# Kernel optimization log

Measured on AMD Instinct MI355X. Metric: run time of the kernel, lower is better.

Reference implementation:

```python
import jax, jax.numpy as jnp
import numpy as np

B, S, D = 4, 2048, 768
H = 12
DH = D // H  # 64


def setup_inputs() -> dict:
    key = jax.random.key(0)
    ks = jax.random.split(key, 6)
    scale = 0.02
    return {
        "hidden_states": jax.random.normal(ks[0], (B, S, D), dtype=jnp.float32),
        "Wq": jax.random.normal(ks[1], (D, D), dtype=jnp.float32) * scale,
        "bq": jnp.zeros((D,), dtype=jnp.float32),
        "Wk": jax.random.normal(ks[2], (D, D), dtype=jnp.float32) * scale,
        "bk": jnp.zeros((D,), dtype=jnp.float32),
        "Wv": jax.random.normal(ks[3], (D, D), dtype=jnp.float32) * scale,
        "bv": jnp.zeros((D,), dtype=jnp.float32),
        "Wo": jax.random.normal(ks[4], (D, D), dtype=jnp.float32) * scale,
        "bo": jnp.zeros((D,), dtype=jnp.float32),
        "w_mix": jnp.ones((2,), dtype=jnp.float32),
    }


def reference(hidden_states, Wq, bq, Wk, bk, Wv, bv, Wo, bo, w_mix):
    # Q/K/V projections, then split heads: [B,S,D] -> [B,H,S,DH]
    def split_heads(x):
        return x.reshape(B, S, H, DH).transpose(0, 2, 1, 3)

    q = split_heads(hidden_states @ Wq.T + bq)
    k = split_heads(hidden_states @ Wk.T + bk)
    v = split_heads(hidden_states @ Wv.T + bv)

    # [B,H,S,S] attention scores
    scores = jnp.einsum("bhqd,bhkd->bhqk", q, k) / jnp.sqrt(jnp.float32(DH))

    attn_soft = jax.nn.softmax(scores, axis=-1)
    attn_relu2 = jnp.square(jax.nn.relu(scores))
    mix = jax.nn.softmax(w_mix)  # exp(w)/sum(exp(w))
    attn = attn_soft * mix[0] + attn_relu2 * mix[1]
    # dropout rate 0.0 (inference) -> identity

    ctx = jnp.einsum("bhqk,bhkd->bhqd", attn, v)
    ctx = ctx.transpose(0, 2, 1, 3).reshape(B, S, D)
    out = ctx @ Wo.T + bo
    return out
```

## Files before the change

kernel.cpp:

```cpp
#include <hip/hip_runtime.h>

#define DEV __device__ __forceinline__

typedef __attribute__((ext_vector_type(8))) short short8;
typedef __attribute__((ext_vector_type(4))) float f32x4;
typedef __attribute__((ext_vector_type(2))) unsigned int u32x2;
typedef __attribute__((ext_vector_type(4))) unsigned int u32x4;

constexpr int Dm = 768;
constexpr int Sn = 2048;
constexpr int Bn = 4;
constexpr int Hn = 12;
constexpr int Mn = Bn * Sn;

constexpr float kQScale = 0.18033688011112043f;
constexpr float kR2Fix  = 0.4804530139182014f;

DEV unsigned short f32_to_bf16(float f) {
  unsigned int u = __float_as_uint(f);
  u = (u + 0x7fffu + ((u >> 16) & 1u)) >> 16;
  return (unsigned short)u;
}

DEV unsigned cvt_pk_bf16(float lo, float hi) {
  unsigned d;
  asm("v_cvt_pk_bf16_f32 %0, %1, %2" : "=v"(d) : "v"(lo), "v"(hi));
  return d;
}

DEV f32x4 mfma_bf16(short8 a, short8 b, f32x4 c) {
  return __builtin_amdgcn_mfma_f32_16x16x32_bf16(a, b, c, 0, 0, 0);
}

DEV void gload_lds16(const void* g, void* l) {
  __builtin_amdgcn_global_load_lds(
      (__attribute__((address_space(1))) const unsigned int*)g,
      (__attribute__((address_space(3))) unsigned int*)l, 16, 0, 0);
}

DEV short8 transpose_to_bfrag(unsigned xd0, unsigned xd1, unsigned yd0, unsigned yd1) {
  u32x2 a0 = __builtin_amdgcn_permlane32_swap(xd0, yd0, false, false);
  u32x2 b0 = __builtin_amdgcn_permlane16_swap(a0[0], a0[1], false, false);
  u32x2 a1 = __builtin_amdgcn_permlane32_swap(xd1, yd1, false, false);
  u32x2 b1 = __builtin_amdgcn_permlane16_swap(a1[0], a1[1], false, false);
  u32x4 f = {b0[0], b1[0], b0[1], b1[1]};
  return __builtin_bit_cast(short8, f);
}

__global__ __launch_bounds__(256) void k_cast_all(
    const float* __restrict__ hs, const float* __restrict__ Wq,
    const float* __restrict__ Wk, const float* __restrict__ Wv,
    const float* __restrict__ Wo, unsigned short* __restrict__ hbf,
    unsigned short* __restrict__ wbf) {
  int bx = blockIdx.x;
  if (bx < 6144) {
    int i = bx * 256 + threadIdx.x;
    float4 v = ((const float4*)hs)[i];
    ushort4 o;
    o.x = f32_to_bf16(v.x); o.y = f32_to_bf16(v.y);
    o.z = f32_to_bf16(v.z); o.w = f32_to_bf16(v.w);
    ((ushort4*)hbf)[i] = o;
  } else {
    int i = (bx - 6144) * 256 + threadIdx.x;
    int w = i / 147456;
    int off = i - w * 147456;
    const float* src = (w == 0) ? Wq : (w == 1) ? Wk : (w == 2) ? Wv : Wo;
    float4 v = ((const float4*)src)[off];
    ushort4 o;
    o.x = f32_to_bf16(v.x); o.y = f32_to_bf16(v.y);
    o.z = f32_to_bf16(v.z); o.w = f32_to_bf16(v.w);
    ((ushort4*)wbf)[w * 147456 + off] = o;
  }
}

__global__ __launch_bounds__(256, 3) void k_gemm_qkv(
    const unsigned short* __restrict__ Abf, const unsigned short* __restrict__ wbf,
    const float* __restrict__ bq, const float* __restrict__ bk, const float* __restrict__ bv,
    unsigned short* __restrict__ Qb, unsigned short* __restrict__ Kb,
    unsigned short* __restrict__ Vt) {
  __shared__ unsigned short Sh[96 * 136];
  unsigned short* As = Sh;
  unsigned short* Bs = Sh + 4096;

  const int tid = threadIdx.x;
  const int wave = tid >> 6, lane = tid & 63;
  const int wm = wave >> 1, wn = wave & 1;
  const int quad = lane >> 4, l16 = lane & 15;
  const int bm = blockIdx.y * 128, bn = blockIdx.x * 192;
  const int seg = blockIdx.x >> 2;
  const int nloc0 = (blockIdx.x & 3) * 192;

  const int sr = lane >> 2;
  const int sc = (lane & 3) * 8;
  const unsigned short* gA0 = Abf + (size_t)(bm + (wave * 2 + 0) * 16 + sr) * Dm + sc;
  const unsigned short* gA1 = Abf + (size_t)(bm + (wave * 2 + 1) * 16 + sr) * Dm + sc;
  const unsigned short* gB0 = wbf + (size_t)(bn + (wave * 3 + 0) * 16 + sr) * Dm + sc;
  const unsigned short* gB1 = wbf + (size_t)(bn + (wave * 3 + 1) * 16 + sr) * Dm + sc;
  const unsigned short* gB2 = wbf + (size_t)(bn + (wave * 3 + 2) * 16 + sr) * Dm + sc;
  unsigned short* lA0 = &As[(wave * 2 + 0) * 512];
  unsigned short* lA1 = &As[(wave * 2 + 1) * 512];
  unsigned short* lB0 = &Bs[(wave * 3 + 0) * 512];
  unsigned short* lB1 = &Bs[(wave * 3 + 1) * 512];
  unsigned short* lB2 = &Bs[(wave * 3 + 2) * 512];

  f32x4 acc[4][6];
#pragma unroll
  for (int i = 0; i < 4; ++i)
#pragma unroll
    for (int j = 0; j < 6; ++j)
#pragma unroll
      for (int r = 0; r < 4; ++r) acc[i][j][r] = 0.f;

  for (int kk = 0; kk < Dm; kk += 32) {
    gload_lds16(gA0 + kk, lA0);
    gload_lds16(gA1 + kk, lA1);
    gload_lds16(gB0 + kk, lB0);
    gload_lds16(gB1 + kk, lB1);
    gload_lds16(gB2 + kk, lB2);
    __syncthreads();
    short8 af[4], bf[6];
#pragma unroll
    for (int mi = 0; mi < 4; ++mi)
      af[mi] = *(const short8*)(&As[(wm * 64 + mi * 16 + l16) * 32 + quad * 8]);
#pragma unroll
    for (int ni = 0; ni < 6; ++ni)
      bf[ni] = *(const short8*)(&Bs[(wn * 96 + ni * 16 + l16) * 32 + quad * 8]);
#pragma unroll
    for (int mi = 0; mi < 4; ++mi)
#pragma unroll
      for (int ni = 0; ni < 6; ++ni)
        acc[mi][ni] = mfma_bf16(af[mi], bf[ni], acc[mi][ni]);
    __syncthreads();
  }

  if (seg != 2) {
    const float* bias = (seg == 0) ? bq : bk;
    unsigned short* Out = (seg == 0) ? Qb : Kb;
    const float scale = (seg == 0) ? kQScale : 1.0f;
#pragma unroll
    for (int ni = 0; ni < 6; ++ni) {
      int n = nloc0 + wn * 96 + ni * 16 + l16;
      float bias_v = bias[n];
#pragma unroll
      for (int mi = 0; mi < 4; ++mi) {
#pragma unroll
        for (int r = 0; r < 4; ++r) {
          int m = bm + wm * 64 + mi * 16 + quad * 4 + r;
          Out[(size_t)m * Dm + n] = f32_to_bf16((acc[mi][ni][r] + bias_v) * scale);
        }
      }
    }
  } else {
    const int bb = bm >> 11;
    const int s0 = bm & 2047;
    const int j = tid >> 4;
    const int cch = tid & 15;
#pragma unroll
    for (int p = 0; p < 2; ++p) {
      if (wn == p) {
#pragma unroll
        for (int ni = 0; ni < 6; ++ni) {
          int nl = ni * 16 + l16;
          float bias_v = bv[nloc0 + p * 96 + nl];
#pragma unroll
          for (int mi = 0; mi < 4; ++mi)
#pragma unroll
            for (int r = 0; r < 4; ++r)
              Sh[nl * 136 + wm * 64 + mi * 16 + quad * 4 + r] =
                  f32_to_bf16(acc[mi][ni][r] + bias_v);
        }
      }
      __syncthreads();
#pragma unroll
      for (int it = 0; it < 6; ++it) {
        int row = it * 16 + j;
        int nv = nloc0 + p * 96 + row;
        int h2 = nv >> 6, dcol = nv & 63;
        uint4 v = *(const uint4*)(&Sh[row * 136 + cch * 8]);
        *(uint4*)(&Vt[((size_t)((bb * Hn + h2) * 64 + dcol)) * Sn + s0 + cch * 8]) = v;
      }
      __syncthreads();
    }
  }
}

__global__ __launch_bounds__(256, 3) void k_attn(
    const unsigned short* __restrict__ Qb, const unsigned short* __restrict__ Kb,
    const unsigned short* __restrict__ Vt, const float* __restrict__ wmix,
    unsigned short* __restrict__ Ctx) {
  __shared__ unsigned short Ks[2][64 * 64];
  __shared__ unsigned short Vs[2][64 * 64];

  const int tid = threadIdx.x;
  const int wave = tid >> 6, lane = tid & 63;
  const int quad = lane >> 4, l16 = lane & 15;
  const int l8 = l16 & 7;
  const int lin = blockIdx.x;
  const int qt = lin / 48;
  const int s = lin % 48;
  const int bh = (s & 7) * 6 + (s >> 3);
  const int b = bh / Hn, h = bh % Hn;

  const unsigned short* Qg = Qb + (size_t)(b * Sn + qt * 128) * Dm + h * 64;
  const unsigned short* Kg = Kb + (size_t)(b * Sn) * Dm + h * 64;
  const unsigned short* Vg = Vt + (size_t)bh * 64 * Sn;

  const int krr = lane >> 3, kcc = lane & 7;
  const int kchunk = kcc ^ krr;

#pragma unroll
  for (int i = 0; i < 4; ++i) {
    int t = wave * 4 + i;
    gload_lds16(Qg + (size_t)(t * 8 + krr) * Dm + kchunk * 8, &Ks[0][0] + t * 512);
  }
  __syncthreads();
  short8 qf[2][2];
#pragma unroll
  for (int mi = 0; mi < 2; ++mi)
#pragma unroll
    for (int ks = 0; ks < 2; ++ks)
      qf[mi][ks] = *(const short8*)(
          &Ks[wave >> 1][((wave & 1) * 32 + mi * 16 + l16) * 64 +
                         (((ks * 4 + quad) ^ l8) << 3)]);
  __syncthreads();

  const f32x4 kZero = {0.f, 0.f, 0.f, 0.f};

  f32x4 acc_s[2][4], acc_r2[2][4];
  float dsum[2];
#pragma unroll
  for (int i = 0; i < 2; ++i) {
#pragma unroll
    for (int j = 0; j < 4; ++j)
#pragma unroll
      for (int r = 0; r < 4; ++r) { acc_s[i][j][r] = 0.f; acc_r2[i][j][r] = 0.f; }
    dsum[i] = 0.f;
  }

#pragma unroll
  for (int i = 0; i < 2; ++i) {
    int t = wave * 2 + i;
    gload_lds16(Kg + (size_t)(t * 8 + krr) * Dm + kchunk * 8, &Ks[0][t * 512]);
    gload_lds16(Vg + (size_t)(t * 8 + krr) * Sn + kchunk * 8, &Vs[0][t * 512]);
  }
  __syncthreads();

  for (int kt = 0; kt < 32; ++kt) {
    const int cur = kt & 1;
    if (kt < 31) {
      const int nxt = cur ^ 1;
      const int kb = (kt + 1) * 64;
#pragma unroll
      for (int i = 0; i < 2; ++i) {
        int t = wave * 2 + i;
        gload_lds16(Kg + (size_t)(kb + t * 8 + krr) * Dm + kchunk * 8, &Ks[nxt][t * 512]);
        gload_lds16(Vg + (size_t)(t * 8 + krr) * Sn + kb + kchunk * 8, &Vs[nxt][t * 512]);
      }
    }

#pragma unroll
    for (int c = 0; c < 2; ++c) {
      short8 kf[2][2];
#pragma unroll
      for (int t2 = 0; t2 < 2; ++t2)
#pragma unroll
        for (int ks = 0; ks < 2; ++ks)
          kf[t2][ks] = *(const short8*)(
              &Ks[cur][(c * 32 + t2 * 16 + l16) * 64 + (((ks * 4 + quad) ^ l8) << 3)]);

      f32x4 sacc[2][2];
#pragma unroll
      for (int mi = 0; mi < 2; ++mi)
#pragma unroll
        for (int t2 = 0; t2 < 2; ++t2)
          sacc[mi][t2] = mfma_bf16(kf[t2][1], qf[mi][1],
                                   mfma_bf16(kf[t2][0], qf[mi][0], kZero));

      short8 vf[4];
#pragma unroll
      for (int nv = 0; nv < 4; ++nv)
        vf[nv] = *(const short8*)(
            &Vs[cur][(nv * 16 + l16) * 64 + (((c * 4 + quad) ^ l8) << 3)]);

#pragma unroll
      for (int mi = 0; mi < 2; ++mi) {
        f32x4 s0 = sacc[mi][0], s1 = sacc[mi][1];
        float p1a[4], p1b[4], p2a[4], p2b[4];
#pragma unroll
        for (int r = 0; r < 4; ++r) {
          p1a[r] = __builtin_amdgcn_exp2f(s0[r]);
          p1b[r] = __builtin_amdgcn_exp2f(s1[r]);
          float t0 = fmaxf(s0[r], 0.f), t1 = fmaxf(s1[r], 0.f);
          p2a[r] = t0 * t0;
          p2b[r] = t1 * t1;
        }
        dsum[mi] += ((p1a[0] + p1a[1]) + (p1a[2] + p1a[3])) +
                    ((p1b[0] + p1b[1]) + (p1b[2] + p1b[3]));
        short8 pf1 = transpose_to_bfrag(cvt_pk_bf16(p1a[0], p1a[1]),
                                        cvt_pk_bf16(p1a[2], p1a[3]),
                                        cvt_pk_bf16(p1b[0], p1b[1]),
                                        cvt_pk_bf16(p1b[2], p1b[3]));
        short8 pf2 = transpose_to_bfrag(cvt_pk_bf16(p2a[0], p2a[1]),
                                        cvt_pk_bf16(p2a[2], p2a[3]),
                                        cvt_pk_bf16(p2b[0], p2b[1]),
                                        cvt_pk_bf16(p2b[2], p2b[3]));
#pragma unroll
        for (int nv = 0; nv < 4; ++nv) {
          acc_s[mi][nv] = mfma_bf16(vf[nv], pf1, acc_s[mi][nv]);
          acc_r2[mi][nv] = mfma_bf16(vf[nv], pf2, acc_r2[mi][nv]);
        }
      }
    }
    __syncthreads();
  }

  float w0 = wmix[0], w1 = wmix[1];
  float e0 = __expf(w0), e1 = __expf(w1);
  float mix0 = e0 / (e0 + e1);
  float mix1 = (e1 / (e0 + e1)) * kR2Fix;

#pragma unroll
  for (int mi = 0; mi < 2; ++mi) {
    float d = dsum[mi];
    d += __shfl_xor(d, 16);
    d += __shfl_xor(d, 32);
    float a0 = mix0 / d;
    int srow = qt * 128 + wave * 32 + mi * 16 + l16;
#pragma unroll
    for (int nv = 0; nv < 4; ++nv) {
      float v0 = fmaf(acc_s[mi][nv][0], a0, mix1 * acc_r2[mi][nv][0]);
      float v1 = fmaf(acc_s[mi][nv][1], a0, mix1 * acc_r2[mi][nv][1]);
      float v2 = fmaf(acc_s[mi][nv][2], a0, mix1 * acc_r2[mi][nv][2]);
      float v3 = fmaf(acc_s[mi][nv][3], a0, mix1 * acc_r2[mi][nv][3]);
      uint2 o;
      o.x = cvt_pk_bf16(v0, v1);
      o.y = cvt_pk_bf16(v2, v3);
      *(uint2*)(&Ctx[(size_t)(b * Sn + srow) * Dm + h * 64 + nv * 16 + quad * 4]) = o;
    }
  }
}

__global__ __launch_bounds__(256, 3) void k_gemm_out(
    const unsigned short* __restrict__ Abf, const unsigned short* __restrict__ W,
    const float* __restrict__ bias, float* __restrict__ out) {
  __shared__ unsigned short As[128 * 32];
  __shared__ unsigned short Bs[128 * 32];

  const int tid = threadIdx.x;
  const int wave = tid >> 6, lane = tid & 63;
  const int wm = wave >> 1, wn = wave & 1;
  const int quad = lane >> 4, l16 = lane & 15;
  const int bm = blockIdx.y * 128, bn = blockIdx.x * 128;

  const int sr = lane >> 2;
  const int sc = (lane & 3) * 8;
  const unsigned short* gA0 = Abf + (size_t)(bm + (wave * 2 + 0) * 16 + sr) * Dm + sc;
  const unsigned short* gA1 = Abf + (size_t)(bm + (wave * 2 + 1) * 16 + sr) * Dm + sc;
  const unsigned short* gB0 = W + (size_t)(bn + (wave * 2 + 0) * 16 + sr) * Dm + sc;
  const unsigned short* gB1 = W + (size_t)(bn + (wave * 2 + 1) * 16 + sr) * Dm + sc;
  unsigned short* lA0 = &As[(wave * 2 + 0) * 512];
  unsigned short* lA1 = &As[(wave * 2 + 1) * 512];
  unsigned short* lB0 = &Bs[(wave * 2 + 0) * 512];
  unsigned short* lB1 = &Bs[(wave * 2 + 1) * 512];

  f32x4 acc[4][4];
#pragma unroll
  for (int i = 0; i < 4; ++i)
#pragma unroll
    for (int j = 0; j < 4; ++j)
#pragma unroll
      for (int r = 0; r < 4; ++r) acc[i][j][r] = 0.f;

  for (int kk = 0; kk < Dm; kk += 32) {
    gload_lds16(gA0 + kk, lA0);
    gload_lds16(gA1 + kk, lA1);
    gload_lds16(gB0 + kk, lB0);
    gload_lds16(gB1 + kk, lB1);
    __syncthreads();
    short8 af[4], bf[4];
#pragma unroll
    for (int mi = 0; mi < 4; ++mi)
      af[mi] = *(const short8*)(&As[(wm * 64 + mi * 16 + l16) * 32 + quad * 8]);
#pragma unroll
    for (int ni = 0; ni < 4; ++ni)
      bf[ni] = *(const short8*)(&Bs[(wn * 64 + ni * 16 + l16) * 32 + quad * 8]);
#pragma unroll
    for (int mi = 0; mi < 4; ++mi)
#pragma unroll
      for (int ni = 0; ni < 4; ++ni)
        acc[mi][ni] = mfma_bf16(af[mi], bf[ni], acc[mi][ni]);
    __syncthreads();
  }

#pragma unroll
  for (int ni = 0; ni < 4; ++ni) {
    int n = bn + wn * 64 + ni * 16 + l16;
    float bias_v = bias[n];
#pragma unroll
    for (int mi = 0; mi < 4; ++mi) {
#pragma unroll
      for (int r = 0; r < 4; ++r) {
        int m = bm + wm * 64 + mi * 16 + quad * 4 + r;
        out[(size_t)m * Dm + n] = acc[mi][ni][r] + bias_v;
      }
    }
  }
}

extern "C" void kernel_launch(void* const* d_in, const int* in_sizes, int n_in,
                              void* d_out, int out_size, void* d_ws, size_t ws_size,
                              hipStream_t stream) {
  const float* hs = (const float*)d_in[0];
  const float* Wq = (const float*)d_in[1];
  const float* bq = (const float*)d_in[2];
  const float* Wk = (const float*)d_in[3];
  const float* bk = (const float*)d_in[4];
  const float* Wv = (const float*)d_in[5];
  const float* bv = (const float*)d_in[6];
  const float* Wo = (const float*)d_in[7];
  const float* bo = (const float*)d_in[8];
  const float* wmix = (const float*)d_in[9];

  unsigned short* hbf = (unsigned short*)d_ws;
  unsigned short* wbf = hbf + (size_t)Mn * Dm;
  unsigned short* Qb  = wbf + (size_t)4 * Dm * Dm;
  unsigned short* Kb  = Qb + (size_t)Mn * Dm;
  unsigned short* Vt  = Kb + (size_t)Mn * Dm;
  unsigned short* Ctx = hbf;

  k_cast_all<<<dim3(8448), dim3(256), 0, stream>>>(hs, Wq, Wk, Wv, Wo, hbf, wbf);
  k_gemm_qkv<<<dim3(12, 64), dim3(256), 0, stream>>>(hbf, wbf, bq, bk, bv, Qb, Kb, Vt);
  k_attn<<<dim3(768), dim3(256), 0, stream>>>(Qb, Kb, Vt, wmix, Ctx);
  k_gemm_out<<<dim3(6, 64), dim3(256), 0, stream>>>(Ctx, wbf + (size_t)3 * Dm * Dm, bo,
                                                    (float*)d_out);
}
```

Before: 246.7 us.

## Split attention block across 8 waves with one 16-row query tile each

The attention kernel now launches 512 threads per block, and each of the 8 waves owns 16 query rows instead of 32. Per-wave accumulators and the Q fragments are halved, which cuts register pressure and raises occupancy (launch bounds 512,4). Each wave loads one K and one V 8-row slice per tile through incremented pointers. In exchange, every K/V fragment read from LDS now feeds only one query sub-tile, so LDS read traffic per MFMA doubles, and the larger block adds synchronization cost.

```diff
diff --git a/kernel.cpp b/kernel.cpp
--- a/kernel.cpp
+++ b/kernel.cpp
@@ -184,7 +184,7 @@
   }
 }
 
-__global__ __launch_bounds__(256, 3) void k_attn(
+__global__ __launch_bounds__(512, 4) void k_attn(
     const unsigned short* __restrict__ Qb, const unsigned short* __restrict__ Kb,
     const unsigned short* __restrict__ Vt, const float* __restrict__ wmix,
     unsigned short* __restrict__ Ctx) {
@@ -209,53 +209,44 @@
   const int kchunk = kcc ^ krr;
 
 #pragma unroll
-  for (int i = 0; i < 4; ++i) {
-    int t = wave * 4 + i;
-    gload_lds16(Qg + (size_t)(t * 8 + krr) * Dm + kchunk * 8, &Ks[0][0] + t * 512);
-  }
-  __syncthreads();
-  short8 qf[2][2];
-#pragma unroll
-  for (int mi = 0; mi < 2; ++mi)
-#pragma unroll
-    for (int ks = 0; ks < 2; ++ks)
-      qf[mi][ks] = *(const short8*)(
-          &Ks[wave >> 1][((wave & 1) * 32 + mi * 16 + l16) * 64 +
-                         (((ks * 4 + quad) ^ l8) << 3)]);
-  __syncthreads();
-
-  const f32x4 kZero = {0.f, 0.f, 0.f, 0.f};
-
-  f32x4 acc_s[2][4], acc_r2[2][4];
-  float dsum[2];
-#pragma unroll
-  for (int i = 0; i < 2; ++i) {
-#pragma unroll
-    for (int j = 0; j < 4; ++j)
-#pragma unroll
-      for (int r = 0; r < 4; ++r) { acc_s[i][j][r] = 0.f; acc_r2[i][j][r] = 0.f; }
-    dsum[i] = 0.f;
-  }
-
-#pragma unroll
   for (int i = 0; i < 2; ++i) {
     int t = wave * 2 + i;
-    gload_lds16(Kg + (size_t)(t * 8 + krr) * Dm + kchunk * 8, &Ks[0][t * 512]);
-    gload_lds16(Vg + (size_t)(t * 8 + krr) * Sn + kchunk * 8, &Vs[0][t * 512]);
-  }
+    gload_lds16(Qg + (size_t)(t * 8 + krr) * Dm + kchunk * 8, &Ks[0][0] + t * 512);
+  }
+  __syncthreads();
+  short8 qf[2];
+  {
+    const unsigned short* qbase = &Ks[0][0] + (wave * 16 + l16) * 64;
+#pragma unroll
+    for (int ks = 0; ks < 2; ++ks)
+      qf[ks] = *(const short8*)(qbase + (((ks * 4 + quad) ^ l8) << 3));
+  }
+  __syncthreads();
+
+  const f32x4 kZero = {0.f, 0.f, 0.f, 0.f};
+
+  f32x4 acc_s[4], acc_r2[4];
+  float dsum = 0.f;
+#pragma unroll
+  for (int j = 0; j < 4; ++j)
+#pragma unroll
+    for (int r = 0; r < 4; ++r) { acc_s[j][r] = 0.f; acc_r2[j][r] = 0.f; }
+
+  const unsigned short* kp = Kg + (size_t)(64 + wave * 8 + krr) * Dm + kchunk * 8;
+  const unsigned short* vp = Vg + (size_t)(wave * 8 + krr) * Sn + 64 + kchunk * 8;
+
+  gload_lds16(Kg + (size_t)(wave * 8 + krr) * Dm + kchunk * 8, &Ks[0][wave * 512]);
+  gload_lds16(Vg + (size_t)(wave * 8 + krr) * Sn + kchunk * 8, &Vs[0][wave * 512]);
   __syncthreads();
 
   for (int kt = 0; kt < 32; ++kt) {
     const int cur = kt & 1;
     if (kt < 31) {
       const int nxt = cur ^ 1;
-      const int kb = (kt + 1) * 64;
-#pragma unroll
-      for (int i = 0; i < 2; ++i) {
-        int t = wave * 2 + i;
-        gload_lds16(Kg + (size_t)(kb + t * 8 + krr) * Dm + kchunk * 8, &Ks[nxt][t * 512]);
-        gload_lds16(Vg + (size_t)(t * 8 + krr) * Sn + kb + kchunk * 8, &Vs[nxt][t * 512]);
-      }
+      gload_lds16(kp, &Ks[nxt][wave * 512]);
+      gload_lds16(vp, &Vs[nxt][wave * 512]);
+      kp += 64 * Dm;
+      vp += 64;
     }
 
 #pragma unroll
@@ -268,13 +259,11 @@
           kf[t2][ks] = *(const short8*)(
               &Ks[cur][(c * 32 + t2 * 16 + l16) * 64 + (((ks * 4 + quad) ^ l8) << 3)]);
 
-      f32x4 sacc[2][2];
-#pragma unroll
-      for (int mi = 0; mi < 2; ++mi)
-#pragma unroll
-        for (int t2 = 0; t2 < 2; ++t2)
-          sacc[mi][t2] = mfma_bf16(kf[t2][1], qf[mi][1],
-                                   mfma_bf16(kf[t2][0], qf[mi][0], kZero));
+      f32x4 sacc[2];
+#pragma unroll
+      for (int t2 = 0; t2 < 2; ++t2)
+        sacc[t2] = mfma_bf16(kf[t2][1], qf[1],
+                             mfma_bf16(kf[t2][0], qf[0], kZero));
 
       short8 vf[4];
 #pragma unroll
@@ -282,33 +271,30 @@
         vf[nv] = *(const short8*)(
             &Vs[cur][(nv * 16 + l16) * 64 + (((c * 4 + quad) ^ l8) << 3)]);
 
-#pragma unroll
-      for (int mi = 0; mi < 2; ++mi) {
-        f32x4 s0 = sacc[mi][0], s1 = sacc[mi][1];
-        float p1a[4], p1b[4], p2a[4], p2b[4];
-#pragma unroll
-        for (int r = 0; r < 4; ++r) {
-          p1a[r] = __builtin_amdgcn_exp2f(s0[r]);
-          p1b[r] = __builtin_amdgcn_exp2f(s1[r]);
-          float t0 = fmaxf(s0[r], 0.f), t1 = fmaxf(s1[r], 0.f);
-          p2a[r] = t0 * t0;
-          p2b[r] = t1 * t1;
-        }
-        dsum[mi] += ((p1a[0] + p1a[1]) + (p1a[2] + p1a[3])) +
-                    ((p1b[0] + p1b[1]) + (p1b[2] + p1b[3]));
-        short8 pf1 = transpose_to_bfrag(cvt_pk_bf16(p1a[0], p1a[1]),
-                                        cvt_pk_bf16(p1a[2], p1a[3]),
-                                        cvt_pk_bf16(p1b[0], p1b[1]),
-                                        cvt_pk_bf16(p1b[2], p1b[3]));
-        short8 pf2 = transpose_to_bfrag(cvt_pk_bf16(p2a[0], p2a[1]),
-                                        cvt_pk_bf16(p2a[2], p2a[3]),
-                                        cvt_pk_bf16(p2b[0], p2b[1]),
-                                        cvt_pk_bf16(p2b[2], p2b[3]));
-#pragma unroll
-        for (int nv = 0; nv < 4; ++nv) {
-          acc_s[mi][nv] = mfma_bf16(vf[nv], pf1, acc_s[mi][nv]);
-          acc_r2[mi][nv] = mfma_bf16(vf[nv], pf2, acc_r2[mi][nv]);
-        }
+      f32x4 s0 = sacc[0], s1 = sacc[1];
+      float p1a[4], p1b[4], p2a[4], p2b[4];
+#pragma unroll
+      for (int r = 0; r < 4; ++r) {
+        p1a[r] = __builtin_amdgcn_exp2f(s0[r]);
+        p1b[r] = __builtin_amdgcn_exp2f(s1[r]);
+        float t0 = fmaxf(s0[r], 0.f), t1 = fmaxf(s1[r], 0.f);
+        p2a[r] = t0 * t0;
+        p2b[r] = t1 * t1;
+      }
+      dsum += ((p1a[0] + p1a[1]) + (p1a[2] + p1a[3])) +
+              ((p1b[0] + p1b[1]) + (p1b[2] + p1b[3]));
+      short8 pf1 = transpose_to_bfrag(cvt_pk_bf16(p1a[0], p1a[1]),
+                                      cvt_pk_bf16(p1a[2], p1a[3]),
+                                      cvt_pk_bf16(p1b[0], p1b[1]),
+                                      cvt_pk_bf16(p1b[2], p1b[3]));
+      short8 pf2 = transpose_to_bfrag(cvt_pk_bf16(p2a[0], p2a[1]),
+                                      cvt_pk_bf16(p2a[2], p2a[3]),
+                                      cvt_pk_bf16(p2b[0], p2b[1]),
+                                      cvt_pk_bf16(p2b[2], p2b[3]));
+#pragma unroll
+      for (int nv = 0; nv < 4; ++nv) {
+        acc_s[nv] = mfma_bf16(vf[nv], pf1, acc_s[nv]);
+        acc_r2[nv] = mfma_bf16(vf[nv], pf2, acc_r2[nv]);
       }
     }
     __syncthreads();
@@ -319,24 +305,21 @@
   float mix0 = e0 / (e0 + e1);
   float mix1 = (e1 / (e0 + e1)) * kR2Fix;
 
-#pragma unroll
-  for (int mi = 0; mi < 2; ++mi) {
-    float d = dsum[mi];
-    d += __shfl_xor(d, 16);
-    d += __shfl_xor(d, 32);
-    float a0 = mix0 / d;
-    int srow = qt * 128 + wave * 32 + mi * 16 + l16;
-#pragma unroll
-    for (int nv = 0; nv < 4; ++nv) {
-      float v0 = fmaf(acc_s[mi][nv][0], a0, mix1 * acc_r2[mi][nv][0]);
-      float v1 = fmaf(acc_s[mi][nv][1], a0, mix1 * acc_r2[mi][nv][1]);
-      float v2 = fmaf(acc_s[mi][nv][2], a0, mix1 * acc_r2[mi][nv][2]);
-      float v3 = fmaf(acc_s[mi][nv][3], a0, mix1 * acc_r2[mi][nv][3]);
-      uint2 o;
-      o.x = cvt_pk_bf16(v0, v1);
-      o.y = cvt_pk_bf16(v2, v3);
-      *(uint2*)(&Ctx[(size_t)(b * Sn + srow) * Dm + h * 64 + nv * 16 + quad * 4]) = o;
-    }
+  float d = dsum;
+  d += __shfl_xor(d, 16);
+  d += __shfl_xor(d, 32);
+  float a0 = mix0 / d;
+  int srow = qt * 128 + wave * 16 + l16;
+#pragma unroll
+  for (int nv = 0; nv < 4; ++nv) {
+    float v0 = fmaf(acc_s[nv][0], a0, mix1 * acc_r2[nv][0]);
+    float v1 = fmaf(acc_s[nv][1], a0, mix1 * acc_r2[nv][1]);
+    float v2 = fmaf(acc_s[nv][2], a0, mix1 * acc_r2[nv][2]);
+    float v3 = fmaf(acc_s[nv][3], a0, mix1 * acc_r2[nv][3]);
+    uint2 o;
+    o.x = cvt_pk_bf16(v0, v1);
+    o.y = cvt_pk_bf16(v2, v3);
+    *(uint2*)(&Ctx[(size_t)(b * Sn + srow) * Dm + h * 64 + nv * 16 + quad * 4]) = o;
   }
 }
 
@@ -430,7 +413,7 @@
 
   k_cast_all<<<dim3(8448), dim3(256), 0, stream>>>(hs, Wq, Wk, Wv, Wo, hbf, wbf);
   k_gemm_qkv<<<dim3(12, 64), dim3(256), 0, stream>>>(hbf, wbf, bq, bk, bv, Qb, Kb, Vt);
-  k_attn<<<dim3(768), dim3(256), 0, stream>>>(Qb, Kb, Vt, wmix, Ctx);
+  k_attn<<<dim3(768), dim3(512), 0, stream>>>(Qb, Kb, Vt, wmix, Ctx);
   k_gemm_out<<<dim3(6, 64), dim3(256), 0, stream>>>(Ctx, wbf + (size_t)3 * Dm * Dm, bo,
                                                     (float*)d_out);
 }
```

After: 257.3 us. 1.04x slower.
